# Optimization experiments

Measured on AMD Instinct MI355X. Metric: run time of the kernel, lower is better.

## Reference

```python
import jax, jax.numpy as jnp
import numpy as np

B, N, DIM, DEPTH, H, DH, MLP = 8, 1024, 768, 6, 12, 64, 3072
INNER = H * DH
LN_EPS = 1e-5


def setup_inputs() -> dict:
    key = jax.random.key(0)
    ks = jax.random.split(key, 8)
    return {
        "x": jax.random.normal(ks[0], (B, N, DIM), jnp.float32),
        "ln1_g": jnp.ones((DEPTH, DIM), jnp.float32),
        "ln1_b": jnp.zeros((DEPTH, DIM), jnp.float32),
        "Wq": jax.random.normal(ks[1], (DEPTH, DIM, INNER), jnp.float32) * 0.02,
        "Wkv": jax.random.normal(ks[2], (DEPTH, DIM, 2 * INNER), jnp.float32) * 0.02,
        "mix_pre": jax.random.normal(ks[3], (DEPTH, H, H), jnp.float32),
        "mix_post": jax.random.normal(ks[4], (DEPTH, H, H), jnp.float32),
        "Wo": jax.random.normal(ks[5], (DEPTH, INNER, DIM), jnp.float32) * 0.02,
        "bo": jnp.zeros((DEPTH, DIM), jnp.float32),
        "s1": jnp.full((DEPTH, DIM), 0.1, jnp.float32),  # LayerScale init_eps for depth<=18
        "ln2_g": jnp.ones((DEPTH, DIM), jnp.float32),
        "ln2_b": jnp.zeros((DEPTH, DIM), jnp.float32),
        "W1": jax.random.normal(ks[6], (DEPTH, DIM, MLP), jnp.float32) * 0.02,
        "b1": jnp.zeros((DEPTH, MLP), jnp.float32),
        "W2": jax.random.normal(ks[7], (DEPTH, MLP, DIM), jnp.float32) * 0.02,
        "b2": jnp.zeros((DEPTH, DIM), jnp.float32),
        "s2": jnp.full((DEPTH, DIM), 0.1, jnp.float32),
    }


def _ln(x, g, b):
    m = jnp.mean(x, axis=-1, keepdims=True)
    v = jnp.mean(jnp.square(x - m), axis=-1, keepdims=True)
    return (x - m) * jax.lax.rsqrt(v + LN_EPS) * g + b


def reference(x, ln1_g, ln1_b, Wq, Wkv, mix_pre, mix_post, Wo, bo, s1,
              ln2_g, ln2_b, W1, b1, W2, b2, s2):
    depth = Wq.shape[0]
    heads = mix_pre.shape[-1]
    dim_head = Wq.shape[-1] // heads
    scale = dim_head ** -0.5
    b_, n_ = x.shape[0], x.shape[1]

    def split_heads(t):  # [b, n, h*d] -> [b, h, n, d]
        return t.reshape(b_, n_, heads, dim_head).transpose(0, 2, 1, 3)

    for i in range(depth):
        # --- talking-heads attention block (PreNorm + LayerScale) ---
        h = _ln(x, ln1_g[i], ln1_b[i])
        q = split_heads(h @ Wq[i])
        kv = h @ Wkv[i]
        k = split_heads(kv[..., : heads * dim_head])
        v = split_heads(kv[..., heads * dim_head:])
        dots = jnp.einsum('bhid,bhjd->bhij', q, k) * scale
        dots = jnp.einsum('bhij,hg->bgij', dots, mix_pre[i])  # pre-softmax head mix
        attn = jax.nn.softmax(dots, axis=-1)
        attn = jnp.einsum('bhij,hg->bgij', attn, mix_post[i])  # post-softmax head mix
        out = jnp.einsum('bhij,bhjd->bhid', attn, v)
        out = out.transpose(0, 2, 1, 3).reshape(b_, n_, heads * dim_head)
        x = (out @ Wo[i] + bo[i]) * s1[i] + x
        # --- feed-forward block (PreNorm + LayerScale) ---
        h = _ln(x, ln2_g[i], ln2_b[i])
        h = jax.nn.gelu(h @ W1[i] + b1[i], approximate=False) @ W2[i] + b2[i]
        x = h * s2[i] + x
    return x
```

## Files before the change

### kernel.cpp

```cpp
#include <hip/hip_runtime.h>

constexpr int kDepth = 6;
constexpr int kB = 8;
constexpr int kN = 1024;
constexpr int kDim = 768;
constexpr int kH = 12;
constexpr int kDh = 64;
constexpr int kMlp = 3072;
constexpr int kRows = kB * kN;
constexpr int kQKV = 2304;

typedef __attribute__((ext_vector_type(4))) float f32x4;
typedef __attribute__((ext_vector_type(8))) short bf16x8;

__device__ __forceinline__ f32x4 mfma16x16x32(bf16x8 a, bf16x8 b, f32x4 c) {
  return __builtin_amdgcn_mfma_f32_16x16x32_bf16(a, b, c, 0, 0, 0);
}

__device__ __forceinline__ unsigned short f2bf(float f) {
  unsigned int u = __builtin_bit_cast(unsigned int, f);
  u = u + 0x7FFFu + ((u >> 16) & 1u);
  return (unsigned short)(u >> 16);
}

__device__ __forceinline__ float bf2f(unsigned short u) {
  return __builtin_bit_cast(float, (unsigned int)u << 16);
}

__device__ __forceinline__ void gload_lds16(const void* g, void* l) {
  __builtin_amdgcn_global_load_lds((__attribute__((address_space(1))) void*)g,
                                   (__attribute__((address_space(3))) void*)l,
                                   16, 0, 0);
}

__global__ __launch_bounds__(256) void ln_kernel(const float* __restrict__ x,
                                                 const float* __restrict__ gamma,
                                                 const float* __restrict__ beta,
                                                 unsigned short* __restrict__ out) {
  int row = blockIdx.x, tid = threadIdx.x;
  const float* xr = x + (size_t)row * kDim;
  float v0 = xr[tid], v1 = xr[tid + 256], v2 = xr[tid + 512];
  float s = v0 + v1 + v2;
  float q = v0 * v0 + v1 * v1 + v2 * v2;
#pragma unroll
  for (int o = 32; o >= 1; o >>= 1) {
    s += __shfl_xor(s, o);
    q += __shfl_xor(q, o);
  }
  __shared__ float ss[4], sq[4];
  int wid = tid >> 6, lane = tid & 63;
  if (lane == 0) { ss[wid] = s; sq[wid] = q; }
  __syncthreads();
  s = ss[0] + ss[1] + ss[2] + ss[3];
  q = sq[0] + sq[1] + sq[2] + sq[3];
  float mean = s * (1.0f / kDim);
  float var = q * (1.0f / kDim) - mean * mean;
  float rstd = rsqrtf(var + 1e-5f);
  unsigned short* orow = out + (size_t)row * kDim;
  orow[tid]       = f2bf((v0 - mean) * rstd * gamma[tid]       + beta[tid]);
  orow[tid + 256] = f2bf((v1 - mean) * rstd * gamma[tid + 256] + beta[tid + 256]);
  orow[tid + 512] = f2bf((v2 - mean) * rstd * gamma[tid + 512] + beta[tid + 512]);
}

__global__ __launch_bounds__(256) void transpose_all(const float* __restrict__ Wq,
                                                     const float* __restrict__ Wkv,
                                                     const float* __restrict__ Wo,
                                                     const float* __restrict__ W1,
                                                     const float* __restrict__ W2,
                                                     unsigned short* __restrict__ wqkvT,
                                                     unsigned short* __restrict__ woT,
                                                     unsigned short* __restrict__ w1T,
                                                     unsigned short* __restrict__ w2T,
                                                     int L) {
  int t = blockIdx.x;
  const float* src;
  unsigned short* dst;
  int R, C, dstOff;
  if (t < 576)       { src = Wq  + (size_t)L * 768 * 768;  R = 768;  C = 768;  dst = wqkvT; dstOff = 0;   }
  else if (t < 1728) { src = Wkv + (size_t)L * 768 * 1536; R = 768;  C = 1536; dst = wqkvT; dstOff = 768; t -= 576; }
  else if (t < 2304) { src = Wo  + (size_t)L * 768 * 768;  R = 768;  C = 768;  dst = woT;   dstOff = 0;   t -= 1728; }
  else if (t < 4608) { src = W1  + (size_t)L * 768 * 3072; R = 768;  C = 3072; dst = w1T;   dstOff = 0;   t -= 2304; }
  else               { src = W2  + (size_t)L * 3072 * 768; R = 3072; C = 768;  dst = w2T;   dstOff = 0;   t -= 4608; }
  int Ct = C >> 5;
  int bx = t % Ct, by = t / Ct;
  __shared__ float tt[32][33];
  int tx = threadIdx.x & 31, ty = threadIdx.x >> 5;
  int c0 = bx * 32, r0 = by * 32;
#pragma unroll
  for (int k = 0; k < 4; ++k) {
    int r = r0 + ty + k * 8;
    tt[ty + k * 8][tx] = src[(size_t)r * C + c0 + tx];
  }
  __syncthreads();
#pragma unroll
  for (int k = 0; k < 4; ++k) {
    int c = c0 + ty + k * 8;
    dst[(size_t)(dstOff + c) * R + r0 + tx] = f2bf(tt[tx][ty + k * 8]);
  }
}

__global__ __launch_bounds__(256) void transpose_v_kernel(const unsigned short* __restrict__ qkv,
                                                          unsigned short* __restrict__ vT) {
  __shared__ unsigned short t[32][33];
  int tx = threadIdx.x & 31, ty = threadIdx.x >> 5;
  int j0 = blockIdx.x * 32, d0 = blockIdx.y * 32;
  int bg = blockIdx.z;
  int b = bg / kH, g = bg % kH;
#pragma unroll
  for (int k = 0; k < 4; ++k) {
    int j = j0 + ty + k * 8;
    t[ty + k * 8][tx] = qkv[(size_t)(b * kN + j) * kQKV + 1536 + g * 64 + d0 + tx];
  }
  __syncthreads();
#pragma unroll
  for (int k = 0; k < 4; ++k) {
    int d = d0 + ty + k * 8;
    vT[((size_t)(b * kH + g) * kDh + d) * kN + j0 + tx] = t[tx][ty + k * 8];
  }
}

template <int EPI>
__global__ __launch_bounds__(256) void gemm_kernel(const unsigned short* __restrict__ A,
                                                   const unsigned short* __restrict__ Bt,
                                                   const float* __restrict__ bias,
                                                   const float* __restrict__ scl,
                                                   float* __restrict__ resid,
                                                   unsigned short* __restrict__ C,
                                                   int K, int ldc) {
  __shared__ __align__(16) unsigned short lA[128 * 64];
  __shared__ __align__(16) unsigned short lB[128 * 64];
  int tid = threadIdx.x, wid = tid >> 6, lane = tid & 63;
  int gx = gridDim.x;
  int nwg = gx * gridDim.y;
  int orig = blockIdx.y * gx + blockIdx.x;
  int chunk = nwg >> 3;
  int wg = (orig & 7) * chunk + (orig >> 3);
  int bx = wg % gx, by = wg / gx;
  int row0 = by * 128, col0 = bx * 128;
  int wr = wid >> 1, wc = wid & 1;
  f32x4 zero = {0.f, 0.f, 0.f, 0.f};
  f32x4 acc[4][4];
#pragma unroll
  for (int m = 0; m < 4; ++m)
#pragma unroll
    for (int n = 0; n < 4; ++n) acc[m][n] = zero;

  for (int kt = 0; kt < K; kt += 64) {
    __syncthreads();
#pragma unroll
    for (int t = 0; t < 4; ++t) {
      int cbase = wid * 256 + t * 64;
      int c = cbase + lane;
      int r = c >> 3, slot = c & 7;
      int k8 = slot ^ (r & 7);
      gload_lds16(&A[(size_t)(row0 + r) * K + kt + k8 * 8], &lA[cbase * 8]);
      gload_lds16(&Bt[(size_t)(col0 + r) * K + kt + k8 * 8], &lB[cbase * 8]);
    }
    __syncthreads();
#pragma unroll
    for (int kk = 0; kk < 2; ++kk) {
      bf16x8 af[4], bfr[4];
      int kslot = kk * 4 + (lane >> 4);
#pragma unroll
      for (int m = 0; m < 4; ++m) {
        int r = wr * 64 + m * 16 + (lane & 15);
        af[m] = *reinterpret_cast<const bf16x8*>(&lA[r * 64 + ((kslot ^ (r & 7)) << 3)]);
      }
#pragma unroll
      for (int n = 0; n < 4; ++n) {
        int r = wc * 64 + n * 16 + (lane & 15);
        bfr[n] = *reinterpret_cast<const bf16x8*>(&lB[r * 64 + ((kslot ^ (r & 7)) << 3)]);
      }
#pragma unroll
      for (int m = 0; m < 4; ++m)
#pragma unroll
        for (int n = 0; n < 4; ++n) acc[m][n] = mfma16x16x32(af[m], bfr[n], acc[m][n]);
    }
  }
#pragma unroll
  for (int m = 0; m < 4; ++m)
#pragma unroll
    for (int n = 0; n < 4; ++n)
#pragma unroll
      for (int r4 = 0; r4 < 4; ++r4) {
        int row = row0 + wr * 64 + m * 16 + ((lane >> 4) << 2) + r4;
        int col = col0 + wc * 64 + n * 16 + (lane & 15);
        float v = acc[m][n][r4];
        if (EPI == 0) {
          C[(size_t)row * ldc + col] = f2bf(v);
        } else if (EPI == 1) {
          v += bias[col];
          v = 0.5f * v * (1.f + erff(v * 0.70710678118654752f));
          C[(size_t)row * ldc + col] = f2bf(v);
        } else {
          v = (v + bias[col]) * scl[col];
          size_t idx = (size_t)row * kDim + col;
          resid[idx] = resid[idx] + v;
        }
      }
}

__global__ __launch_bounds__(256) void dots_kernel(const unsigned short* __restrict__ qkv,
                                                   unsigned short* __restrict__ dots,
                                                   int i0, int IC) {
  constexpr int TROW = 24;
  __shared__ __align__(16) unsigned short T[32 * 32 * TROW];
  int tid = threadIdx.x, wid = tid >> 6, lane = tid & 63;
  int kg = lane >> 4, l15 = lane & 15;
  int j0 = blockIdx.x * 32;
  int il0 = blockIdx.y * 32;
  int b = blockIdx.z;
  for (int idx = tid; idx < 2048; idx += 256) {
    int pos = idx >> 1;
    *(unsigned int*)&T[pos * TROW + 12 + (idx & 1) * 2] = 0u;
  }
  f32x4 zero = {0.f, 0.f, 0.f, 0.f};
#pragma unroll
  for (int rep = 0; rep < 3; ++rep) {
    int h = rep * 4 + wid;
    f32x4 acc[2][2];
    acc[0][0] = zero; acc[0][1] = zero; acc[1][0] = zero; acc[1][1] = zero;
#pragma unroll
    for (int kk = 0; kk < 2; ++kk) {
      bf16x8 aq[2], bk[2];
#pragma unroll
      for (int m = 0; m < 2; ++m) {
        int tok = i0 + il0 + m * 16 + l15;
        aq[m] = *reinterpret_cast<const bf16x8*>(
            &qkv[(size_t)(b * kN + tok) * kQKV + h * 64 + kk * 32 + kg * 8]);
      }
#pragma unroll
      for (int n = 0; n < 2; ++n) {
        int tj = j0 + n * 16 + l15;
        bk[n] = *reinterpret_cast<const bf16x8*>(
            &qkv[(size_t)(b * kN + tj) * kQKV + 768 + h * 64 + kk * 32 + kg * 8]);
      }
#pragma unroll
      for (int m = 0; m < 2; ++m)
#pragma unroll
        for (int n = 0; n < 2; ++n) acc[m][n] = mfma16x16x32(aq[m], bk[n], acc[m][n]);
    }
#pragma unroll
    for (int m = 0; m < 2; ++m)
#pragma unroll
      for (int n = 0; n < 2; ++n)
#pragma unroll
        for (int r = 0; r < 4; ++r)
          T[((m * 16 + kg * 4 + r) * 32 + n * 16 + l15) * TROW + h] = f2bf(acc[m][n][r]);
  }
  __syncthreads();
#pragma unroll
  for (int k = 0; k < 8; ++k) {
    int c = tid + k * 256;
    int pos = c >> 1, half = c & 1;
    int ii = pos >> 5, jj = pos & 31;
    *(f32x4*)&dots[((size_t)(b * IC + il0 + ii) * kN + j0 + jj) * 16 + half * 8] =
        *(const f32x4*)&T[pos * TROW + half * 8];
  }
}

__global__ __launch_bounds__(256) void softmax_mix_kernel(const unsigned short* __restrict__ dots,
                                                          const float* __restrict__ pre,
                                                          const float* __restrict__ post,
                                                          unsigned short* __restrict__ pbuf,
                                                          int IC) {
  constexpr int EROW = 24;
  __shared__ __align__(16) unsigned short E[1024 * EROW];
  __shared__ __align__(16) unsigned short preA[16 * 32];
  __shared__ __align__(16) unsigned short postA[16 * 32];
  __shared__ float red[4][16];
  __shared__ float lgs[16];
  int tid = threadIdx.x, wid = tid >> 6, lane = tid & 63;
  int kg = lane >> 4, l15 = lane & 15;
  int i = blockIdx.x, b = blockIdx.y;
  for (int idx = tid; idx < 512; idx += 256) {
    int m = idx >> 5, k = idx & 31;
    preA[idx] = f2bf((m < 12 && k < 12) ? pre[k * 12 + m] * 0.125f : 0.f);
  }
  __syncthreads();
  bf16x8 preF = *(const bf16x8*)&preA[l15 * 32 + kg * 8];
  const unsigned short* drow = dots + (size_t)(b * IC + i) * kN * 16;
  f32x4 zero = {0.f, 0.f, 0.f, 0.f};
  bf16x8 zfrag = {0, 0, 0, 0, 0, 0, 0, 0};
  float psum[4] = {0.f, 0.f, 0.f, 0.f};
#pragma unroll
  for (int grp = 0; grp < 16; ++grp) {
    int j = wid * 256 + grp * 16 + l15;
    bf16x8 bfrag = (kg < 2) ? *(const bf16x8*)&drow[(size_t)j * 16 + kg * 8] : zfrag;
    f32x4 d = mfma16x16x32(preF, bfrag, zero);
    float ee[4];
#pragma unroll
    for (int r = 0; r < 4; ++r) {
      float dc = fminf(fmaxf(d[r], -15.f), 15.f);
      ee[r] = (kg == 3) ? 0.f : __expf(dc);
      psum[r] += ee[r];
    }
    unsigned int w0, w1;
    asm("v_cvt_pk_bf16_f32 %0, %1, %2" : "=v"(w0) : "v"(ee[0]), "v"(ee[1]));
    asm("v_cvt_pk_bf16_f32 %0, %1, %2" : "=v"(w1) : "v"(ee[2]), "v"(ee[3]));
    *(unsigned int*)&E[j * EROW + kg * 4] = w0;
    *(unsigned int*)&E[j * EROW + kg * 4 + 2] = w1;
  }
#pragma unroll
  for (int r = 0; r < 4; ++r) {
    psum[r] += __shfl_xor(psum[r], 1);
    psum[r] += __shfl_xor(psum[r], 2);
    psum[r] += __shfl_xor(psum[r], 4);
    psum[r] += __shfl_xor(psum[r], 8);
  }
  if (l15 == 0) {
#pragma unroll
    for (int r = 0; r < 4; ++r) red[wid][kg * 4 + r] = psum[r];
  }
  __syncthreads();
  if (tid < 16) {
    float s = red[0][tid] + red[1][tid] + red[2][tid] + red[3][tid];
    lgs[tid] = (tid < 12) ? 1.f / s : 0.f;
  }
  __syncthreads();
  for (int idx = tid; idx < 512; idx += 256) {
    int m = idx >> 5, k = idx & 31;
    postA[idx] = f2bf((m < 12 && k < 12) ? post[k * 12 + m] * lgs[k] : 0.f);
  }
  __syncthreads();
  bf16x8 postF = *(const bf16x8*)&postA[l15 * 32 + kg * 8];
#pragma unroll
  for (int grp = 0; grp < 16; ++grp) {
    int j = wid * 256 + grp * 16 + l15;
    bf16x8 efrag = (kg < 2) ? *(const bf16x8*)&E[j * EROW + kg * 8] : zfrag;
    f32x4 d2 = mfma16x16x32(postF, efrag, zero);
    if (kg < 3) {
#pragma unroll
      for (int r = 0; r < 4; ++r) {
        int g2 = kg * 4 + r;
        pbuf[((size_t)(b * kH + g2) * IC + i) * kN + j] = f2bf(d2[r]);
      }
    }
  }
}

__global__ __launch_bounds__(256) void pv_kernel(const unsigned short* __restrict__ pbuf,
                                                 const unsigned short* __restrict__ vT,
                                                 unsigned short* __restrict__ attn_out,
                                                 int i0, int IC) {
  int tid = threadIdx.x, wid = tid >> 6, lane = tid & 63;
  int kg = lane >> 4, l15 = lane & 15;
  int i32 = blockIdx.x * 32;
  int g = blockIdx.y, b = blockIdx.z;
  const unsigned short* prow = pbuf + (size_t)(b * kH + g) * IC * kN;
  const unsigned short* vrow = vT + (size_t)(b * kH + g) * kDh * kN;
  f32x4 zero = {0.f, 0.f, 0.f, 0.f};
  f32x4 acc[2][4];
#pragma unroll
  for (int half = 0; half < 2; ++half)
#pragma unroll
    for (int n = 0; n < 4; ++n) acc[half][n] = zero;
#pragma unroll
  for (int s = 0; s < 8; ++s) {
    int kt = (wid * 8 + s) * 32 + kg * 8;
    bf16x8 ap[2];
#pragma unroll
    for (int half = 0; half < 2; ++half)
      ap[half] = *reinterpret_cast<const bf16x8*>(&prow[(size_t)(i32 + half * 16 + l15) * kN + kt]);
#pragma unroll
    for (int n = 0; n < 4; ++n) {
      bf16x8 bv = *reinterpret_cast<const bf16x8*>(&vrow[(size_t)(n * 16 + l15) * kN + kt]);
#pragma unroll
      for (int half = 0; half < 2; ++half)
        acc[half][n] = mfma16x16x32(ap[half], bv, acc[half][n]);
    }
  }
  __shared__ float red[3][32][64];
  if (wid > 0) {
#pragma unroll
    for (int half = 0; half < 2; ++half)
#pragma unroll
      for (int n = 0; n < 4; ++n)
#pragma unroll
        for (int r = 0; r < 4; ++r)
          red[wid - 1][half * 16 + kg * 4 + r][n * 16 + l15] = acc[half][n][r];
  }
  __syncthreads();
  if (wid == 0) {
#pragma unroll
    for (int half = 0; half < 2; ++half)
#pragma unroll
      for (int n = 0; n < 4; ++n)
#pragma unroll
        for (int r = 0; r < 4; ++r) {
          int rr = half * 16 + kg * 4 + r, cc = n * 16 + l15;
          float v = acc[half][n][r] + red[0][rr][cc] + red[1][rr][cc] + red[2][rr][cc];
          int tok = i0 + i32 + rr;
          attn_out[(size_t)(b * kN + tok) * kDim + g * kDh + cc] = f2bf(v);
        }
  }
}

extern "C" void kernel_launch(void* const* d_in, const int* in_sizes, int n_in,
                              void* d_out, int out_size, void* d_ws, size_t ws_size,
                              hipStream_t stream) {
  (void)in_sizes; (void)n_in; (void)out_size;
  const float* x     = (const float*)d_in[0];
  const float* ln1_g = (const float*)d_in[1];
  const float* ln1_b = (const float*)d_in[2];
  const float* Wq    = (const float*)d_in[3];
  const float* Wkv   = (const float*)d_in[4];
  const float* pre   = (const float*)d_in[5];
  const float* post  = (const float*)d_in[6];
  const float* Wo    = (const float*)d_in[7];
  const float* bo    = (const float*)d_in[8];
  const float* s1    = (const float*)d_in[9];
  const float* ln2_g = (const float*)d_in[10];
  const float* ln2_b = (const float*)d_in[11];
  const float* W1    = (const float*)d_in[12];
  const float* b1    = (const float*)d_in[13];
  const float* W2    = (const float*)d_in[14];
  const float* b2    = (const float*)d_in[15];
  const float* s2    = (const float*)d_in[16];
  float* xo = (float*)d_out;

  char* ws = (char*)d_ws;
  size_t off = 0;
  auto alloc = [&](size_t bytes) -> void* {
    void* p = ws + off;
    off += (bytes + 255) & ~(size_t)255;
    return p;
  };
  unsigned short* h_buf   = (unsigned short*)alloc((size_t)kRows * kDim * 2);
  unsigned short* qkv     = (unsigned short*)alloc((size_t)kRows * kQKV * 2);
  unsigned short* vT      = (unsigned short*)alloc((size_t)kB * kH * kDh * kN * 2);
  unsigned short* attnout = (unsigned short*)alloc((size_t)kRows * kDim * 2);
  unsigned short* mid     = (unsigned short*)alloc((size_t)kRows * kMlp * 2);
  unsigned short* wqkvT   = (unsigned short*)alloc((size_t)kQKV * kDim * 2);
  unsigned short* woT     = (unsigned short*)alloc((size_t)kDim * kDim * 2);
  unsigned short* w1T     = (unsigned short*)alloc((size_t)kMlp * kDim * 2);
  unsigned short* w2T     = (unsigned short*)alloc((size_t)kDim * kMlp * 2);

  size_t base = off;
  int IC = 1024;
  while (IC > 32 && base + (size_t)IC * (262144 + 196608) + 1024 > ws_size) IC >>= 1;
  unsigned short* dots = (unsigned short*)alloc((size_t)kB * IC * kN * 16 * 2);
  unsigned short* pbuf = (unsigned short*)alloc((size_t)kB * kH * IC * kN * 2);

  hipMemcpyAsync(xo, x, (size_t)kRows * kDim * 4, hipMemcpyDeviceToDevice, stream);

  for (int L = 0; L < kDepth; ++L) {
    ln_kernel<<<kRows, 256, 0, stream>>>(xo, ln1_g + L * kDim, ln1_b + L * kDim, h_buf);
    transpose_all<<<6912, 256, 0, stream>>>(Wq, Wkv, Wo, W1, W2, wqkvT, woT, w1T, w2T, L);

    gemm_kernel<0><<<dim3(kQKV / 128, kRows / 128), 256, 0, stream>>>(
        h_buf, wqkvT, nullptr, nullptr, nullptr, qkv, kDim, kQKV);
    transpose_v_kernel<<<dim3(kN / 32, kDh / 32, kB * kH), 256, 0, stream>>>(qkv, vT);

    for (int i0 = 0; i0 < kN; i0 += IC) {
      dots_kernel<<<dim3(kN / 32, IC / 32, kB), 256, 0, stream>>>(qkv, dots, i0, IC);
      softmax_mix_kernel<<<dim3(IC, kB), 256, 0, stream>>>(
          dots, pre + L * 144, post + L * 144, pbuf, IC);
      pv_kernel<<<dim3(IC / 32, kH, kB), 256, 0, stream>>>(pbuf, vT, attnout, i0, IC);
    }
    gemm_kernel<2><<<dim3(kDim / 128, kRows / 128), 256, 0, stream>>>(
        attnout, woT, bo + L * kDim, s1 + L * kDim, xo, nullptr, kDim, kDim);

    ln_kernel<<<kRows, 256, 0, stream>>>(xo, ln2_g + L * kDim, ln2_b + L * kDim, h_buf);
    gemm_kernel<1><<<dim3(kMlp / 128, kRows / 128), 256, 0, stream>>>(
        h_buf, w1T, b1 + L * kMlp, nullptr, nullptr, mid, kDim, kMlp);
    gemm_kernel<2><<<dim3(kDim / 128, kRows / 128), 256, 0, stream>>>(
        mid, w2T, b2 + L * kDim, s2 + L * kDim, xo, nullptr, kMlp, kDim);
  }
}
```

Measured before the change: 3.528 ms.

## Batch all-layer weight transposes and use 64-row tiles for residual GEMMs

All six layers' weights are now transposed and converted to bf16 in a single launch before the layer loop, instead of one launch per layer. Per-layer pointers index into enlarged weight buffers. The two N=768 residual-update GEMMs move to a new kernel with 64x128 tiles, which doubles the workgroup count from 384 to 768 to fill the GPU's compute units better. The cost is extra workspace for all-layer weight copies and less reuse per tile in those GEMMs.

```diff
diff --git a/kernel.cpp b/kernel.cpp
--- a/kernel.cpp
+++ b/kernel.cpp
@@ -62,25 +62,26 @@
   orow[tid + 512] = f2bf((v2 - mean) * rstd * gamma[tid + 512] + beta[tid + 512]);
 }
 
-__global__ __launch_bounds__(256) void transpose_all(const float* __restrict__ Wq,
-                                                     const float* __restrict__ Wkv,
-                                                     const float* __restrict__ Wo,
-                                                     const float* __restrict__ W1,
-                                                     const float* __restrict__ W2,
-                                                     unsigned short* __restrict__ wqkvT,
-                                                     unsigned short* __restrict__ woT,
-                                                     unsigned short* __restrict__ w1T,
-                                                     unsigned short* __restrict__ w2T,
-                                                     int L) {
+__global__ __launch_bounds__(256) void transpose_all6(const float* __restrict__ Wq,
+                                                      const float* __restrict__ Wkv,
+                                                      const float* __restrict__ Wo,
+                                                      const float* __restrict__ W1,
+                                                      const float* __restrict__ W2,
+                                                      unsigned short* __restrict__ wqkvT,
+                                                      unsigned short* __restrict__ woT,
+                                                      unsigned short* __restrict__ w1T,
+                                                      unsigned short* __restrict__ w2T) {
   int t = blockIdx.x;
+  int L = t / 6912;
+  t -= L * 6912;
   const float* src;
   unsigned short* dst;
   int R, C, dstOff;
-  if (t < 576)       { src = Wq  + (size_t)L * 768 * 768;  R = 768;  C = 768;  dst = wqkvT; dstOff = 0;   }
-  else if (t < 1728) { src = Wkv + (size_t)L * 768 * 1536; R = 768;  C = 1536; dst = wqkvT; dstOff = 768; t -= 576; }
-  else if (t < 2304) { src = Wo  + (size_t)L * 768 * 768;  R = 768;  C = 768;  dst = woT;   dstOff = 0;   t -= 1728; }
-  else if (t < 4608) { src = W1  + (size_t)L * 768 * 3072; R = 768;  C = 3072; dst = w1T;   dstOff = 0;   t -= 2304; }
-  else               { src = W2  + (size_t)L * 3072 * 768; R = 3072; C = 768;  dst = w2T;   dstOff = 0;   t -= 4608; }
+  if (t < 576)       { src = Wq  + (size_t)L * 768 * 768;  R = 768;  C = 768;  dst = wqkvT + (size_t)L * kQKV * kDim; dstOff = 0;   }
+  else if (t < 1728) { src = Wkv + (size_t)L * 768 * 1536; R = 768;  C = 1536; dst = wqkvT + (size_t)L * kQKV * kDim; dstOff = 768; t -= 576; }
+  else if (t < 2304) { src = Wo  + (size_t)L * 768 * 768;  R = 768;  C = 768;  dst = woT  + (size_t)L * kDim * kDim;  dstOff = 0;   t -= 1728; }
+  else if (t < 4608) { src = W1  + (size_t)L * 768 * 3072; R = 768;  C = 3072; dst = w1T  + (size_t)L * kMlp * kDim;  dstOff = 0;   t -= 2304; }
+  else               { src = W2  + (size_t)L * 3072 * 768; R = 3072; C = 768;  dst = w2T  + (size_t)L * kDim * kMlp;  dstOff = 0;   t -= 4608; }
   int Ct = C >> 5;
   int bx = t % Ct, by = t / Ct;
   __shared__ float tt[32][33];
@@ -123,8 +124,6 @@
 __global__ __launch_bounds__(256) void gemm_kernel(const unsigned short* __restrict__ A,
                                                    const unsigned short* __restrict__ Bt,
                                                    const float* __restrict__ bias,
-                                                   const float* __restrict__ scl,
-                                                   float* __restrict__ resid,
                                                    unsigned short* __restrict__ C,
                                                    int K, int ldc) {
   __shared__ __align__(16) unsigned short lA[128 * 64];
@@ -188,15 +187,86 @@
         float v = acc[m][n][r4];
         if (EPI == 0) {
           C[(size_t)row * ldc + col] = f2bf(v);
-        } else if (EPI == 1) {
+        } else {
           v += bias[col];
           v = 0.5f * v * (1.f + erff(v * 0.70710678118654752f));
           C[(size_t)row * ldc + col] = f2bf(v);
-        } else {
-          v = (v + bias[col]) * scl[col];
-          size_t idx = (size_t)row * kDim + col;
-          resid[idx] = resid[idx] + v;
         }
+      }
+}
+
+__global__ __launch_bounds__(256) void gemm64_kernel(const unsigned short* __restrict__ A,
+                                                     const unsigned short* __restrict__ Bt,
+                                                     const float* __restrict__ bias,
+                                                     const float* __restrict__ scl,
+                                                     float* __restrict__ resid,
+                                                     int K) {
+  __shared__ __align__(16) unsigned short lA[64 * 64];
+  __shared__ __align__(16) unsigned short lB[128 * 64];
+  int tid = threadIdx.x, wid = tid >> 6, lane = tid & 63;
+  int gx = gridDim.x;
+  int nwg = gx * gridDim.y;
+  int orig = blockIdx.y * gx + blockIdx.x;
+  int chunk = nwg >> 3;
+  int wg = (orig & 7) * chunk + (orig >> 3);
+  int bx = wg % gx, by = wg / gx;
+  int row0 = by * 64, col0 = bx * 128;
+  int wr = wid & 1, wc = wid >> 1;
+  f32x4 zero = {0.f, 0.f, 0.f, 0.f};
+  f32x4 acc[2][4];
+#pragma unroll
+  for (int m = 0; m < 2; ++m)
+#pragma unroll
+    for (int n = 0; n < 4; ++n) acc[m][n] = zero;
+
+  for (int kt = 0; kt < K; kt += 64) {
+    __syncthreads();
+#pragma unroll
+    for (int t = 0; t < 2; ++t) {
+      int c = t * 256 + tid;
+      int r = c >> 3, slot = c & 7;
+      int k8 = slot ^ (r & 7);
+      gload_lds16(&A[(size_t)(row0 + r) * K + kt + k8 * 8], &lA[c * 8]);
+    }
+#pragma unroll
+    for (int t = 0; t < 4; ++t) {
+      int c = t * 256 + tid;
+      int r = c >> 3, slot = c & 7;
+      int k8 = slot ^ (r & 7);
+      gload_lds16(&Bt[(size_t)(col0 + r) * K + kt + k8 * 8], &lB[c * 8]);
+    }
+    __syncthreads();
+#pragma unroll
+    for (int kk = 0; kk < 2; ++kk) {
+      bf16x8 af[2], bfr[4];
+      int kslot = kk * 4 + (lane >> 4);
+#pragma unroll
+      for (int m = 0; m < 2; ++m) {
+        int r = wr * 32 + m * 16 + (lane & 15);
+        af[m] = *reinterpret_cast<const bf16x8*>(&lA[r * 64 + ((kslot ^ (r & 7)) << 3)]);
+      }
+#pragma unroll
+      for (int n = 0; n < 4; ++n) {
+        int r = wc * 64 + n * 16 + (lane & 15);
+        bfr[n] = *reinterpret_cast<const bf16x8*>(&lB[r * 64 + ((kslot ^ (r & 7)) << 3)]);
+      }
+#pragma unroll
+      for (int m = 0; m < 2; ++m)
+#pragma unroll
+        for (int n = 0; n < 4; ++n) acc[m][n] = mfma16x16x32(af[m], bfr[n], acc[m][n]);
+    }
+  }
+#pragma unroll
+  for (int m = 0; m < 2; ++m)
+#pragma unroll
+    for (int n = 0; n < 4; ++n)
+#pragma unroll
+      for (int r4 = 0; r4 < 4; ++r4) {
+        int row = row0 + wr * 32 + m * 16 + ((lane >> 4) << 2) + r4;
+        int col = col0 + wc * 64 + n * 16 + (lane & 15);
+        float v = (acc[m][n][r4] + bias[col]) * scl[col];
+        size_t idx = (size_t)row * kDim + col;
+        resid[idx] = resid[idx] + v;
       }
 }
 
@@ -431,10 +501,10 @@
   unsigned short* vT      = (unsigned short*)alloc((size_t)kB * kH * kDh * kN * 2);
   unsigned short* attnout = (unsigned short*)alloc((size_t)kRows * kDim * 2);
   unsigned short* mid     = (unsigned short*)alloc((size_t)kRows * kMlp * 2);
-  unsigned short* wqkvT   = (unsigned short*)alloc((size_t)kQKV * kDim * 2);
-  unsigned short* woT     = (unsigned short*)alloc((size_t)kDim * kDim * 2);
-  unsigned short* w1T     = (unsigned short*)alloc((size_t)kMlp * kDim * 2);
-  unsigned short* w2T     = (unsigned short*)alloc((size_t)kDim * kMlp * 2);
+  unsigned short* wqkvT   = (unsigned short*)alloc((size_t)kDepth * kQKV * kDim * 2);
+  unsigned short* woT     = (unsigned short*)alloc((size_t)kDepth * kDim * kDim * 2);
+  unsigned short* w1T     = (unsigned short*)alloc((size_t)kDepth * kMlp * kDim * 2);
+  unsigned short* w2T     = (unsigned short*)alloc((size_t)kDepth * kDim * kMlp * 2);
 
   size_t base = off;
   int IC = 1024;
@@ -443,13 +513,17 @@
   unsigned short* pbuf = (unsigned short*)alloc((size_t)kB * kH * IC * kN * 2);
 
   hipMemcpyAsync(xo, x, (size_t)kRows * kDim * 4, hipMemcpyDeviceToDevice, stream);
+  transpose_all6<<<6 * 6912, 256, 0, stream>>>(Wq, Wkv, Wo, W1, W2, wqkvT, woT, w1T, w2T);
 
   for (int L = 0; L < kDepth; ++L) {
+    const unsigned short* wqkvL = wqkvT + (size_t)L * kQKV * kDim;
+    const unsigned short* woL   = woT   + (size_t)L * kDim * kDim;
+    const unsigned short* w1L   = w1T   + (size_t)L * kMlp * kDim;
+    const unsigned short* w2L   = w2T   + (size_t)L * kDim * kMlp;
+
     ln_kernel<<<kRows, 256, 0, stream>>>(xo, ln1_g + L * kDim, ln1_b + L * kDim, h_buf);
-    transpose_all<<<6912, 256, 0, stream>>>(Wq, Wkv, Wo, W1, W2, wqkvT, woT, w1T, w2T, L);
-
     gemm_kernel<0><<<dim3(kQKV / 128, kRows / 128), 256, 0, stream>>>(
-        h_buf, wqkvT, nullptr, nullptr, nullptr, qkv, kDim, kQKV);
+        h_buf, wqkvL, nullptr, qkv, kDim, kQKV);
     transpose_v_kernel<<<dim3(kN / 32, kDh / 32, kB * kH), 256, 0, stream>>>(qkv, vT);
 
     for (int i0 = 0; i0 < kN; i0 += IC) {
@@ -458,13 +532,13 @@
           dots, pre + L * 144, post + L * 144, pbuf, IC);
       pv_kernel<<<dim3(IC / 32, kH, kB), 256, 0, stream>>>(pbuf, vT, attnout, i0, IC);
     }
-    gemm_kernel<2><<<dim3(kDim / 128, kRows / 128), 256, 0, stream>>>(
-        attnout, woT, bo + L * kDim, s1 + L * kDim, xo, nullptr, kDim, kDim);
+    gemm64_kernel<<<dim3(kDim / 128, kRows / 64), 256, 0, stream>>>(
+        attnout, woL, bo + L * kDim, s1 + L * kDim, xo, kDim);
 
     ln_kernel<<<kRows, 256, 0, stream>>>(xo, ln2_g + L * kDim, ln2_b + L * kDim, h_buf);
     gemm_kernel<1><<<dim3(kMlp / 128, kRows / 128), 256, 0, stream>>>(
-        h_buf, w1T, b1 + L * kMlp, nullptr, nullptr, mid, kDim, kMlp);
-    gemm_kernel<2><<<dim3(kDim / 128, kRows / 128), 256, 0, stream>>>(
-        mid, w2T, b2 + L * kDim, s2 + L * kDim, xo, nullptr, kMlp, kDim);
-  }
-}
+        h_buf, w1L, b1 + L * kMlp, mid, kDim, kMlp);
+    gemm64_kernel<<<dim3(kDim / 128, kRows / 64), 256, 0, stream>>>(
+        mid, w2L, b2 + L * kDim, s2 + L * kDim, xo, kMlp);
+  }
+}
```

New measurement: 4.402 ms. 24.8% more time.
